# Performance work log

Hardware: AMD Instinct MI355X
Metric: run time of the kernel (lower is better)

Reference implementation:

```python
import jax, jax.numpy as jnp
import numpy as np

N = 50000      # nodes
E = 500000     # edges (before self-loops)
D_IN = 128     # embedding_dim
C = 256        # intermediate_dim (per-head out channels)
H = 1          # heads
SLOPE = 0.2    # LeakyReLU negative slope (PyG default)


def setup_inputs() -> dict:
    key = jax.random.key(0)
    ks = jax.random.split(key, 8)
    x = jax.random.normal(ks[0], (N, D_IN), dtype=jnp.float32)
    edge_index = jax.random.randint(ks[1], (2, E), 0, N, dtype=jnp.int32)
    W1 = jax.random.normal(ks[2], (H * C, D_IN), dtype=jnp.float32) / np.sqrt(D_IN)
    a1_src = jax.random.normal(ks[3], (H, C), dtype=jnp.float32) / np.sqrt(C)
    a1_dst = jax.random.normal(ks[4], (H, C), dtype=jnp.float32) / np.sqrt(C)
    b1 = jnp.zeros((C,), dtype=jnp.float32)
    W2 = jax.random.normal(ks[5], (H * C, C), dtype=jnp.float32) / np.sqrt(C)
    a2_src = jax.random.normal(ks[6], (H, C), dtype=jnp.float32) / np.sqrt(C)
    a2_dst = jax.random.normal(ks[7], (H, C), dtype=jnp.float32) / np.sqrt(C)
    b2 = jnp.zeros((C,), dtype=jnp.float32)
    return dict(x=x, edge_index=edge_index, W1=W1, a1_src=a1_src, a1_dst=a1_dst,
                b1=b1, W2=W2, a2_src=a2_src, a2_dst=a2_dst, b2=b2)


def gat_conv(x, src, dst, W, a_src, a_dst, b):
    # x: [N, Din]; W: [H*C, Din]; a_*: [H, C]; b: [C]
    h = (x @ W.T).reshape(N, H, C)                      # [N, H, C]
    e_src = jnp.einsum('nhc,hc->nh', h, a_src)          # [N, H]
    e_dst = jnp.einsum('nhc,hc->nh', h, a_dst)          # [N, H]
    e = jax.nn.leaky_relu(e_src[src] + e_dst[dst], SLOPE)  # [Etot, H]
    # segment softmax over destination nodes (self-loops guarantee >=1 edge per node)
    m = jax.lax.stop_gradient(jax.ops.segment_max(e, dst, num_segments=N))
    p = jnp.exp(e - m[dst])                             # [Etot, H]
    denom = jax.ops.segment_sum(p, dst, num_segments=N)  # [N, H]
    alpha = p / (denom[dst] + 1e-16)                    # [Etot, H]
    out = jax.ops.segment_sum(h[src] * alpha[:, :, None], dst, num_segments=N)  # [N, H, C]
    return out.mean(axis=1) + b                         # concat=False -> head mean; [N, C]


def reference(x, edge_index, W1, a1_src, a1_dst, b1, W2, a2_src, a2_dst, b2):
    # PyG GATConv default add_self_loops=True
    loop = jnp.arange(N, dtype=edge_index.dtype)
    src = jnp.concatenate([edge_index[0], loop])
    dst = jnp.concatenate([edge_index[1], loop])
    x1 = jax.nn.relu(gat_conv(x, src, dst, W1, a1_src, a1_dst, b1))
    x2 = jax.nn.relu(gat_conv(x1, src, dst, W2, a2_src, a2_dst, b2))
    return jnp.concatenate([x1, x2], axis=-1)           # [N, 2*C]
```

## Files before the change

kernel.cpp:

```cpp
#include <hip/hip_runtime.h>
#include <hip/hip_bf16.h>
#include <math.h>

#define NNODES 50000
#define NEDGES 500000
#define ETOT   (NEDGES + NNODES)
#define DIN    128
#define CH     256
#define SLOPE  0.2f

#define SCAN_TILE 1024
#define NSCAN ((NNODES + SCAN_TILE - 1) / SCAN_TILE)

typedef __attribute__((ext_vector_type(8))) short short8;
typedef __attribute__((ext_vector_type(4))) float f32x4;

static __device__ __forceinline__ float wave_reduce_max(float v) {
#pragma unroll
  for (int off = 32; off > 0; off >>= 1) v = fmaxf(v, __shfl_xor(v, off));
  return v;
}
static __device__ __forceinline__ float wave_reduce_sum(float v) {
#pragma unroll
  for (int off = 32; off > 0; off >>= 1) v += __shfl_xor(v, off);
  return v;
}

static __device__ __forceinline__ unsigned short f2bf(float f) {
  unsigned int u = __float_as_uint(f);
  unsigned int r = (u + 0x7fffu + ((u >> 16) & 1u)) >> 16;
  return (unsigned short)r;
}
static __device__ __forceinline__ float bf2f(unsigned short u) {
  return __uint_as_float(((unsigned int)u) << 16);
}

__global__ __launch_bounds__(256) void init_kernel(int* __restrict__ deg,
                                                   float* __restrict__ eS1, float* __restrict__ eD1,
                                                   float* __restrict__ eS2, float* __restrict__ eD2) {
  int i = blockIdx.x * 256 + threadIdx.x;
  if (i < NNODES) {
    deg[i] = 0;
    eS1[i] = 0.f; eD1[i] = 0.f;
    eS2[i] = 0.f; eD2[i] = 0.f;
  }
}

__global__ void degree_kernel(const int* __restrict__ ei, int* __restrict__ deg) {
  int e = blockIdx.x * blockDim.x + threadIdx.x;
  if (e >= ETOT) return;
  int dst = (e < NEDGES) ? ei[NEDGES + e] : (e - NEDGES);
  atomicAdd(&deg[dst], 1);
}

__global__ __launch_bounds__(256) void scan_blocksums(const int* __restrict__ deg,
                                                      int* __restrict__ bsums) {
  __shared__ int sdata[4];
  int b = blockIdx.x;
  int tid = threadIdx.x;
  int idx = b * SCAN_TILE + tid * 4;
  int s = 0;
  if (idx + 3 < NNODES) {
    int4 v = *(const int4*)(deg + idx);
    s = v.x + v.y + v.z + v.w;
  } else {
#pragma unroll
    for (int j = 0; j < 4; j++) if (idx + j < NNODES) s += deg[idx + j];
  }
#pragma unroll
  for (int off = 32; off > 0; off >>= 1) s += __shfl_xor(s, off);
  if ((tid & 63) == 0) sdata[tid >> 6] = s;
  __syncthreads();
  if (tid == 0) bsums[b] = sdata[0] + sdata[1] + sdata[2] + sdata[3];
}

__global__ __launch_bounds__(64) void scan_bsums(const int* __restrict__ bsums,
                                                 int* __restrict__ boffs,
                                                 int* __restrict__ rowptr) {
  int tid = threadIdx.x;
  int v = (tid < NSCAN) ? bsums[tid] : 0;
  int x = v;
#pragma unroll
  for (int off = 1; off < 64; off <<= 1) {
    int t = __shfl_up(x, off);
    if (tid >= off) x += t;
  }
  if (tid < NSCAN) boffs[tid] = x - v;
  if (tid == 63) rowptr[NNODES] = x;
}

__global__ __launch_bounds__(256) void scan_final(const int* __restrict__ deg,
                                                  const int* __restrict__ boffs,
                                                  int* __restrict__ rowptr,
                                                  int* __restrict__ cursor) {
  __shared__ int wsums[4];
  int b = blockIdx.x;
  int tid = threadIdx.x;
  int lane = tid & 63;
  int base = b * SCAN_TILE + tid * 4;
  int d[4];
  int s = 0;
#pragma unroll
  for (int j = 0; j < 4; j++) {
    d[j] = (base + j < NNODES) ? deg[base + j] : 0;
    s += d[j];
  }
  int x = s;
#pragma unroll
  for (int off = 1; off < 64; off <<= 1) {
    int t = __shfl_up(x, off);
    if (lane >= off) x += t;
  }
  if (lane == 63) wsums[tid >> 6] = x;
  __syncthreads();
  int woff = 0;
  int w = tid >> 6;
  for (int i = 0; i < w; i++) woff += wsums[i];
  int excl = boffs[b] + woff + (x - s);
#pragma unroll
  for (int j = 0; j < 4; j++) {
    if (base + j < NNODES) { rowptr[base + j] = excl; cursor[base + j] = excl; }
    excl += d[j];
  }
}

__global__ void scatter_kernel(const int* __restrict__ ei, int* __restrict__ cursor,
                               int* __restrict__ csr_src) {
  int e = blockIdx.x * blockDim.x + threadIdx.x;
  if (e >= ETOT) return;
  int src, dst;
  if (e < NEDGES) { src = ei[e]; dst = ei[NEDGES + e]; }
  else            { src = e - NEDGES; dst = src; }
  int slot = atomicAdd(&cursor[dst], 1);
  csr_src[slot] = src;
}

#define W1N4 (CH * DIN / 4)
#define W2N4 (CH * CH / 4)
__global__ __launch_bounds__(256) void cast_weights(const float* __restrict__ W1,
                                                    const float* __restrict__ W2,
                                                    unsigned short* __restrict__ Wb1,
                                                    unsigned short* __restrict__ Wb2) {
  int i = blockIdx.x * 256 + threadIdx.x;
  const float* src;
  unsigned short* dst;
  int j;
  if (i < W1N4) { src = W1; dst = Wb1; j = i; }
  else if (i < W1N4 + W2N4) { src = W2; dst = Wb2; j = i - W1N4; }
  else return;
  float4 v = *(const float4*)(src + (size_t)j * 4);
  ushort4 o;
  o.x = f2bf(v.x); o.y = f2bf(v.y); o.z = f2bf(v.z); o.w = f2bf(v.w);
  *(ushort4*)(dst + (size_t)j * 4) = o;
}

#define TM 128
#define TN 128
#define TK 64
#define LDA (TK + 8)
#define LDC (TN + 8)

__global__ __launch_bounds__(256) void gemm_bf16(
    const float* __restrict__ Xf, const unsigned short* __restrict__ Xb, int ldx,
    const unsigned short* __restrict__ W, int K,
    unsigned short* __restrict__ Hout, int M,
    const float* __restrict__ a_src, const float* __restrict__ a_dst,
    float* __restrict__ eS, float* __restrict__ eD) {
  __shared__ short smem[TM * LDA * 2];
  short* As = smem;
  short* Bs = smem + TM * LDA;
  short* Cs = smem;
  int bm = blockIdx.y * TM;
  int bn = blockIdx.x * TN;
  int tid = threadIdx.x;
  int wid = tid >> 6;
  int lane = tid & 63;
  int wm = (wid & 1) * 64;
  int wn = (wid >> 1) * 64;
  int lrow = lane & 15;
  int lk8 = (lane >> 4) * 8;

  int srow = tid >> 3;
  int skoff = (tid & 7) * 8;

  f32x4 acc[4][4] = {};

  for (int k0 = 0; k0 < K; k0 += TK) {
#pragma unroll
    for (int i = 0; i < 4; i++) {
      int r = srow + 32 * i;
      int gm = bm + r;
      short8 v = {};
      if (gm < M) {
        if (Xf) {
          const float* p = Xf + (size_t)gm * ldx + k0 + skoff;
          float4 f0 = *(const float4*)(p);
          float4 f1 = *(const float4*)(p + 4);
          v[0] = (short)f2bf(f0.x); v[1] = (short)f2bf(f0.y);
          v[2] = (short)f2bf(f0.z); v[3] = (short)f2bf(f0.w);
          v[4] = (short)f2bf(f1.x); v[5] = (short)f2bf(f1.y);
          v[6] = (short)f2bf(f1.z); v[7] = (short)f2bf(f1.w);
        } else {
          v = *(const short8*)(Xb + (size_t)gm * ldx + k0 + skoff);
        }
      }
      *(short8*)(&As[r * LDA + skoff]) = v;
      short8 w = *(const short8*)(W + (size_t)(bn + r) * K + k0 + skoff);
      *(short8*)(&Bs[r * LDA + skoff]) = w;
    }
    __syncthreads();
#pragma unroll
    for (int kk = 0; kk < TK; kk += 32) {
      short8 a[4], b[4];
#pragma unroll
      for (int mi = 0; mi < 4; mi++)
        a[mi] = *(const short8*)(&As[(wm + mi * 16 + lrow) * LDA + kk + lk8]);
#pragma unroll
      for (int ni = 0; ni < 4; ni++)
        b[ni] = *(const short8*)(&Bs[(wn + ni * 16 + lrow) * LDA + kk + lk8]);
#pragma unroll
      for (int mi = 0; mi < 4; mi++)
#pragma unroll
        for (int ni = 0; ni < 4; ni++)
          acc[mi][ni] = __builtin_amdgcn_mfma_f32_16x16x32_bf16(a[mi], b[ni], acc[mi][ni], 0, 0, 0);
    }
    __syncthreads();
  }

  int crow = (lane >> 4) * 4;
  int ccol = lane & 15;

  float asv[4], adv[4];
#pragma unroll
  for (int ni = 0; ni < 4; ni++) {
    int c = bn + wn + ni * 16 + ccol;
    asv[ni] = a_src[c];
    adv[ni] = a_dst[c];
  }
#pragma unroll
  for (int mi = 0; mi < 4; mi++) {
#pragma unroll
    for (int r = 0; r < 4; r++) {
      float s = 0.f, d = 0.f;
#pragma unroll
      for (int ni = 0; ni < 4; ni++) {
        float h = acc[mi][ni][r];
        s += h * asv[ni];
        d += h * adv[ni];
      }
#pragma unroll
      for (int off = 1; off < 16; off <<= 1) {
        s += __shfl_xor(s, off);
        d += __shfl_xor(d, off);
      }
      int gm = bm + wm + mi * 16 + crow + r;
      if (ccol == 0 && gm < M) {
        atomicAdd(&eS[gm], s);
        atomicAdd(&eD[gm], d);
      }
    }
  }

#pragma unroll
  for (int mi = 0; mi < 4; mi++) {
#pragma unroll
    for (int ni = 0; ni < 4; ni++) {
#pragma unroll
      for (int r = 0; r < 4; r++) {
        int row = wm + mi * 16 + crow + r;
        int col = wn + ni * 16 + ccol;
        Cs[row * LDC + col] = (short)f2bf(acc[mi][ni][r]);
      }
    }
  }
  __syncthreads();
  int orow = tid >> 4;
  int ocol = (tid & 15) * 8;
#pragma unroll
  for (int pp = 0; pp < 8; pp++) {
    int row = pp * 16 + orow;
    int gm = bm + row;
    if (gm < M) {
      short8 v = *(const short8*)(&Cs[row * LDC + ocol]);
      *(short8*)(&Hout[(size_t)gm * CH + bn + ocol]) = v;
    }
  }
}

__global__ __launch_bounds__(256) void aggregate_kernel(
    const unsigned short* __restrict__ Hmb, const float* __restrict__ eS,
    const float* __restrict__ eD, const int* __restrict__ rowptr,
    const int* __restrict__ csr_src, const float* __restrict__ bias,
    float* __restrict__ out, int outOffset, unsigned short* __restrict__ xout) {
  int n = blockIdx.x * 4 + (threadIdx.x >> 6);
  if (n >= NNODES) return;
  int lane = threadIdx.x & 63;
  int beg = rowptr[n], end = rowptr[n + 1];
  int deg = end - beg;
  float ed = eD[n];

  float4 acc = make_float4(0.f, 0.f, 0.f, 0.f);

  if (deg <= 64) {
    int src = 0;
    float e = -1e30f;
    if (lane < deg) {
      src = csr_src[beg + lane];
      float t = eS[src] + ed;
      e = (t >= 0.f) ? t : SLOPE * t;
    }
    float m = wave_reduce_max(e);
    float p = (lane < deg) ? __expf(e - m) : 0.f;
    float inv = 1.f / (wave_reduce_sum(p) + 1e-16f);

    for (int j0 = 0; j0 < deg; j0 += 8) {
      ushort4 hv[8];
      float al[8];
#pragma unroll
      for (int t = 0; t < 8; t++) {
        int j = j0 + t;
        int jj = (j < deg) ? j : deg - 1;
        int sj = __shfl(src, jj);
        float aj = __shfl(p, jj) * inv;
        al[t] = (j < deg) ? aj : 0.f;
        hv[t] = *(const ushort4*)(Hmb + (size_t)sj * CH + lane * 4);
      }
#pragma unroll
      for (int t = 0; t < 8; t++) {
        acc.x += al[t] * bf2f(hv[t].x);
        acc.y += al[t] * bf2f(hv[t].y);
        acc.z += al[t] * bf2f(hv[t].z);
        acc.w += al[t] * bf2f(hv[t].w);
      }
    }
  } else {
    float m = -1e30f;
    for (int i = lane; i < deg; i += 64) {
      float e = eS[csr_src[beg + i]] + ed;
      e = (e >= 0.f) ? e : SLOPE * e;
      m = fmaxf(m, e);
    }
    m = wave_reduce_max(m);
    float ds = 0.f;
    for (int i = lane; i < deg; i += 64) {
      float e = eS[csr_src[beg + i]] + ed;
      e = (e >= 0.f) ? e : SLOPE * e;
      ds += __expf(e - m);
    }
    ds = wave_reduce_sum(ds) + 1e-16f;
    float inv = 1.f / ds;
    for (int k = beg; k < end; k++) {
      int s = csr_src[k];
      float e = eS[s] + ed;
      e = (e >= 0.f) ? e : SLOPE * e;
      float alpha = __expf(e - m) * inv;
      ushort4 hu = *(const ushort4*)(Hmb + (size_t)s * CH + lane * 4);
      acc.x += alpha * bf2f(hu.x); acc.y += alpha * bf2f(hu.y);
      acc.z += alpha * bf2f(hu.z); acc.w += alpha * bf2f(hu.w);
    }
  }

  float4 b = *(const float4*)(bias + lane * 4);
  float4 o;
  o.x = fmaxf(acc.x + b.x, 0.f);
  o.y = fmaxf(acc.y + b.y, 0.f);
  o.z = fmaxf(acc.z + b.z, 0.f);
  o.w = fmaxf(acc.w + b.w, 0.f);
  *(float4*)(out + (size_t)n * 512 + outOffset + lane * 4) = o;
  if (xout) {
    ushort4 ob;
    ob.x = f2bf(o.x); ob.y = f2bf(o.y); ob.z = f2bf(o.z); ob.w = f2bf(o.w);
    *(ushort4*)(xout + (size_t)n * CH + lane * 4) = ob;
  }
}

extern "C" void kernel_launch(void* const* d_in, const int* in_sizes, int n_in,
                              void* d_out, int out_size, void* d_ws, size_t ws_size,
                              hipStream_t stream) {
  const float* x   = (const float*)d_in[0];
  const int*   ei  = (const int*)d_in[1];
  const float* W1  = (const float*)d_in[2];
  const float* a1s = (const float*)d_in[3];
  const float* a1d = (const float*)d_in[4];
  const float* b1  = (const float*)d_in[5];
  const float* W2  = (const float*)d_in[6];
  const float* a2s = (const float*)d_in[7];
  const float* a2d = (const float*)d_in[8];
  const float* b2  = (const float*)d_in[9];
  float* out = (float*)d_out;

  char* ws = (char*)d_ws;
  size_t off = 0;
  auto alloc = [&](size_t bytes) -> void* {
    void* p = ws + off;
    off = (off + bytes + 255) & ~(size_t)255;
    return p;
  };
  unsigned short* Hmb    = (unsigned short*)alloc(sizeof(short) * (size_t)NNODES * CH);
  unsigned short* Xb     = (unsigned short*)alloc(sizeof(short) * (size_t)NNODES * CH);
  unsigned short* Wb1    = (unsigned short*)alloc(sizeof(short) * CH * DIN);
  unsigned short* Wb2    = (unsigned short*)alloc(sizeof(short) * CH * CH);
  float*          eS1    = (float*)alloc(sizeof(float) * NNODES);
  float*          eD1    = (float*)alloc(sizeof(float) * NNODES);
  float*          eS2    = (float*)alloc(sizeof(float) * NNODES);
  float*          eD2    = (float*)alloc(sizeof(float) * NNODES);
  int*            rowptr = (int*)alloc(sizeof(int) * (NNODES + 1));
  int*            cursor = (int*)alloc(sizeof(int) * NNODES);
  int*            csrsrc = (int*)alloc(sizeof(int) * ETOT);
  int*            deg    = (int*)alloc(sizeof(int) * NNODES);
  int*            bsums  = (int*)alloc(sizeof(int) * NSCAN);
  int*            boffs  = (int*)alloc(sizeof(int) * NSCAN);

  init_kernel<<<(NNODES + 255) / 256, 256, 0, stream>>>(deg, eS1, eD1, eS2, eD2);
  cast_weights<<<(W1N4 + W2N4 + 255) / 256, 256, 0, stream>>>(W1, W2, Wb1, Wb2);

  degree_kernel<<<(ETOT + 255) / 256, 256, 0, stream>>>(ei, deg);
  scan_blocksums<<<NSCAN, 256, 0, stream>>>(deg, bsums);
  scan_bsums<<<1, 64, 0, stream>>>(bsums, boffs, rowptr);
  scan_final<<<NSCAN, 256, 0, stream>>>(deg, boffs, rowptr, cursor);
  scatter_kernel<<<(ETOT + 255) / 256, 256, 0, stream>>>(ei, cursor, csrsrc);

  dim3 gemm_grid(2, (NNODES + TM - 1) / TM);
  int nblk4 = (NNODES + 3) / 4;

  gemm_bf16<<<gemm_grid, 256, 0, stream>>>(x, (const unsigned short*)nullptr, DIN,
                                           Wb1, DIN, Hmb, NNODES, a1s, a1d, eS1, eD1);
  aggregate_kernel<<<nblk4, 256, 0, stream>>>(Hmb, eS1, eD1, rowptr, csrsrc, b1, out, 0, Xb);

  gemm_bf16<<<gemm_grid, 256, 0, stream>>>((const float*)nullptr, Xb, CH,
                                           Wb2, CH, Hmb, NNODES, a2s, a2d, eS2, eD2);
  aggregate_kernel<<<nblk4, 256, 0, stream>>>(Hmb, eS2, eD2, rowptr, csrsrc, b2, out, 256, (unsigned short*)nullptr);
}
```

Baseline: 335.6 us.

## Fuse init/cast and degree-count into GEMM launch; split aggregation into half-wave edges

Merges the zero-init and weight-cast kernels into one launch. It also folds the edge degree-count into the first GEMM launch as extra blocks, so the counting overlaps the GEMM and launches are removed. The aggregation kernel now has each half-wave process a different edge using 16-byte row loads of 8 bf16 channels, then combines the halves with a cross-lane shuffle. This is meant to cut gather instruction count and raise memory-level parallelism, at the cost of more registers and a final reduction.

After: 330.2 us. No clear change (-1.6%).

```diff
diff --git a/kernel.cpp b/kernel.cpp
--- a/kernel.cpp
+++ b/kernel.cpp
@@ -35,22 +35,31 @@
   return __uint_as_float(((unsigned int)u) << 16);
 }
 
-__global__ __launch_bounds__(256) void init_kernel(int* __restrict__ deg,
-                                                   float* __restrict__ eS1, float* __restrict__ eD1,
-                                                   float* __restrict__ eS2, float* __restrict__ eD2) {
+#define W1N4 (CH * DIN / 4)
+#define W2N4 (CH * CH / 4)
+__global__ __launch_bounds__(256) void init_and_cast(
+    int* __restrict__ deg,
+    float* __restrict__ eS1, float* __restrict__ eD1,
+    float* __restrict__ eS2, float* __restrict__ eD2,
+    const float* __restrict__ W1, const float* __restrict__ W2,
+    unsigned short* __restrict__ Wb1, unsigned short* __restrict__ Wb2) {
   int i = blockIdx.x * 256 + threadIdx.x;
   if (i < NNODES) {
     deg[i] = 0;
     eS1[i] = 0.f; eD1[i] = 0.f;
     eS2[i] = 0.f; eD2[i] = 0.f;
   }
-}
-
-__global__ void degree_kernel(const int* __restrict__ ei, int* __restrict__ deg) {
-  int e = blockIdx.x * blockDim.x + threadIdx.x;
-  if (e >= ETOT) return;
-  int dst = (e < NEDGES) ? ei[NEDGES + e] : (e - NEDGES);
-  atomicAdd(&deg[dst], 1);
+  if (i < W1N4 + W2N4) {
+    const float* src;
+    unsigned short* dst;
+    int j;
+    if (i < W1N4) { src = W1; dst = Wb1; j = i; }
+    else          { src = W2; dst = Wb2; j = i - W1N4; }
+    float4 v = *(const float4*)(src + (size_t)j * 4);
+    ushort4 o;
+    o.x = f2bf(v.x); o.y = f2bf(v.y); o.z = f2bf(v.z); o.w = f2bf(v.w);
+    *(ushort4*)(dst + (size_t)j * 4) = o;
+  }
 }
 
 __global__ __launch_bounds__(256) void scan_blocksums(const int* __restrict__ deg,
@@ -135,43 +144,25 @@
   csr_src[slot] = src;
 }
 
-#define W1N4 (CH * DIN / 4)
-#define W2N4 (CH * CH / 4)
-__global__ __launch_bounds__(256) void cast_weights(const float* __restrict__ W1,
-                                                    const float* __restrict__ W2,
-                                                    unsigned short* __restrict__ Wb1,
-                                                    unsigned short* __restrict__ Wb2) {
-  int i = blockIdx.x * 256 + threadIdx.x;
-  const float* src;
-  unsigned short* dst;
-  int j;
-  if (i < W1N4) { src = W1; dst = Wb1; j = i; }
-  else if (i < W1N4 + W2N4) { src = W2; dst = Wb2; j = i - W1N4; }
-  else return;
-  float4 v = *(const float4*)(src + (size_t)j * 4);
-  ushort4 o;
-  o.x = f2bf(v.x); o.y = f2bf(v.y); o.z = f2bf(v.z); o.w = f2bf(v.w);
-  *(ushort4*)(dst + (size_t)j * 4) = o;
-}
-
 #define TM 128
 #define TN 128
 #define TK 64
 #define LDA (TK + 8)
 #define LDC (TN + 8)
-
-__global__ __launch_bounds__(256) void gemm_bf16(
+#define GEMM_GRID (2 * ((NNODES + TM - 1) / TM))
+#define DEG_BLOCKS ((ETOT + 255) / 256)
+
+static __device__ __forceinline__ void gemm_body(
     const float* __restrict__ Xf, const unsigned short* __restrict__ Xb, int ldx,
     const unsigned short* __restrict__ W, int K,
     unsigned short* __restrict__ Hout, int M,
     const float* __restrict__ a_src, const float* __restrict__ a_dst,
-    float* __restrict__ eS, float* __restrict__ eD) {
+    float* __restrict__ eS, float* __restrict__ eD,
+    int bm, int bn) {
   __shared__ short smem[TM * LDA * 2];
   short* As = smem;
   short* Bs = smem + TM * LDA;
   short* Cs = smem;
-  int bm = blockIdx.y * TM;
-  int bn = blockIdx.x * TN;
   int tid = threadIdx.x;
   int wid = tid >> 6;
   int lane = tid & 63;
@@ -287,6 +278,37 @@
   }
 }
 
+__global__ __launch_bounds__(256) void gemm1_deg(
+    const float* __restrict__ Xf, const unsigned short* __restrict__ W,
+    unsigned short* __restrict__ Hout,
+    const float* __restrict__ a_src, const float* __restrict__ a_dst,
+    float* __restrict__ eS, float* __restrict__ eD,
+    const int* __restrict__ ei, int* __restrict__ deg) {
+  if (blockIdx.x >= GEMM_GRID) {
+    int e = (blockIdx.x - GEMM_GRID) * 256 + threadIdx.x;
+    if (e < ETOT) {
+      int dst = (e < NEDGES) ? ei[NEDGES + e] : (e - NEDGES);
+      atomicAdd(&deg[dst], 1);
+    }
+    return;
+  }
+  int bn = (blockIdx.x & 1) * TN;
+  int bm = (blockIdx.x >> 1) * TM;
+  gemm_body(Xf, (const unsigned short*)nullptr, DIN, W, DIN, Hout, NNODES,
+            a_src, a_dst, eS, eD, bm, bn);
+}
+
+__global__ __launch_bounds__(256) void gemm_l2(
+    const unsigned short* __restrict__ Xb, const unsigned short* __restrict__ W,
+    unsigned short* __restrict__ Hout,
+    const float* __restrict__ a_src, const float* __restrict__ a_dst,
+    float* __restrict__ eS, float* __restrict__ eD) {
+  int bn = blockIdx.x * TN;
+  int bm = blockIdx.y * TM;
+  gemm_body((const float*)nullptr, Xb, CH, W, CH, Hout, NNODES,
+            a_src, a_dst, eS, eD, bm, bn);
+}
+
 __global__ __launch_bounds__(256) void aggregate_kernel(
     const unsigned short* __restrict__ Hmb, const float* __restrict__ eS,
     const float* __restrict__ eD, const int* __restrict__ rowptr,
@@ -295,11 +317,15 @@
   int n = blockIdx.x * 4 + (threadIdx.x >> 6);
   if (n >= NNODES) return;
   int lane = threadIdx.x & 63;
+  int half = lane >> 5;
+  int cg = lane & 31;
   int beg = rowptr[n], end = rowptr[n + 1];
   int deg = end - beg;
   float ed = eD[n];
 
-  float4 acc = make_float4(0.f, 0.f, 0.f, 0.f);
+  float acc8[8];
+#pragma unroll
+  for (int k = 0; k < 8; k++) acc8[k] = 0.f;
 
   if (deg <= 64) {
     int src = 0;
@@ -312,25 +338,30 @@
     float m = wave_reduce_max(e);
     float p = (lane < deg) ? __expf(e - m) : 0.f;
     float inv = 1.f / (wave_reduce_sum(p) + 1e-16f);
-
-    for (int j0 = 0; j0 < deg; j0 += 8) {
-      ushort4 hv[8];
+    float av = p * inv;
+
+    for (int j0 = 0; j0 < deg; j0 += 16) {
+      uint4 hv[8];
       float al[8];
 #pragma unroll
       for (int t = 0; t < 8; t++) {
-        int j = j0 + t;
+        int j = j0 + 2 * t + half;
         int jj = (j < deg) ? j : deg - 1;
         int sj = __shfl(src, jj);
-        float aj = __shfl(p, jj) * inv;
+        float aj = __shfl(av, jj);
         al[t] = (j < deg) ? aj : 0.f;
-        hv[t] = *(const ushort4*)(Hmb + (size_t)sj * CH + lane * 4);
+        hv[t] = *(const uint4*)(Hmb + (size_t)sj * CH + cg * 8);
       }
 #pragma unroll
       for (int t = 0; t < 8; t++) {
-        acc.x += al[t] * bf2f(hv[t].x);
-        acc.y += al[t] * bf2f(hv[t].y);
-        acc.z += al[t] * bf2f(hv[t].z);
-        acc.w += al[t] * bf2f(hv[t].w);
+        acc8[0] += al[t] * __uint_as_float(hv[t].x << 16);
+        acc8[1] += al[t] * __uint_as_float(hv[t].x & 0xffff0000u);
+        acc8[2] += al[t] * __uint_as_float(hv[t].y << 16);
+        acc8[3] += al[t] * __uint_as_float(hv[t].y & 0xffff0000u);
+        acc8[4] += al[t] * __uint_as_float(hv[t].z << 16);
+        acc8[5] += al[t] * __uint_as_float(hv[t].z & 0xffff0000u);
+        acc8[6] += al[t] * __uint_as_float(hv[t].w << 16);
+        acc8[7] += al[t] * __uint_as_float(hv[t].w & 0xffff0000u);
       }
     }
   } else {
@@ -347,30 +378,45 @@
       e = (e >= 0.f) ? e : SLOPE * e;
       ds += __expf(e - m);
     }
-    ds = wave_reduce_sum(ds) + 1e-16f;
-    float inv = 1.f / ds;
-    for (int k = beg; k < end; k++) {
+    float inv = 1.f / (wave_reduce_sum(ds) + 1e-16f);
+    for (int j = 0; j < deg; j += 2) {
+      int jj = j + half;
+      int k = beg + ((jj < deg) ? jj : deg - 1);
       int s = csr_src[k];
       float e = eS[s] + ed;
       e = (e >= 0.f) ? e : SLOPE * e;
-      float alpha = __expf(e - m) * inv;
-      ushort4 hu = *(const ushort4*)(Hmb + (size_t)s * CH + lane * 4);
-      acc.x += alpha * bf2f(hu.x); acc.y += alpha * bf2f(hu.y);
-      acc.z += alpha * bf2f(hu.z); acc.w += alpha * bf2f(hu.w);
-    }
-  }
-
-  float4 b = *(const float4*)(bias + lane * 4);
+      float alpha = (jj < deg) ? __expf(e - m) * inv : 0.f;
+      uint4 u = *(const uint4*)(Hmb + (size_t)s * CH + cg * 8);
+      acc8[0] += alpha * __uint_as_float(u.x << 16);
+      acc8[1] += alpha * __uint_as_float(u.x & 0xffff0000u);
+      acc8[2] += alpha * __uint_as_float(u.y << 16);
+      acc8[3] += alpha * __uint_as_float(u.y & 0xffff0000u);
+      acc8[4] += alpha * __uint_as_float(u.z << 16);
+      acc8[5] += alpha * __uint_as_float(u.z & 0xffff0000u);
+      acc8[6] += alpha * __uint_as_float(u.w << 16);
+      acc8[7] += alpha * __uint_as_float(u.w & 0xffff0000u);
+    }
+  }
+
+#pragma unroll
+  for (int k = 0; k < 8; k++) acc8[k] += __shfl_xor(acc8[k], 32);
+
+  float a0 = half ? acc8[4] : acc8[0];
+  float a1 = half ? acc8[5] : acc8[1];
+  float a2 = half ? acc8[6] : acc8[2];
+  float a3 = half ? acc8[7] : acc8[3];
+  int cbase = cg * 8 + half * 4;
+  float4 b = *(const float4*)(bias + cbase);
   float4 o;
-  o.x = fmaxf(acc.x + b.x, 0.f);
-  o.y = fmaxf(acc.y + b.y, 0.f);
-  o.z = fmaxf(acc.z + b.z, 0.f);
-  o.w = fmaxf(acc.w + b.w, 0.f);
-  *(float4*)(out + (size_t)n * 512 + outOffset + lane * 4) = o;
+  o.x = fmaxf(a0 + b.x, 0.f);
+  o.y = fmaxf(a1 + b.y, 0.f);
+  o.z = fmaxf(a2 + b.z, 0.f);
+  o.w = fmaxf(a3 + b.w, 0.f);
+  *(float4*)(out + (size_t)n * 512 + outOffset + cbase) = o;
   if (xout) {
     ushort4 ob;
     ob.x = f2bf(o.x); ob.y = f2bf(o.y); ob.z = f2bf(o.z); ob.w = f2bf(o.w);
-    *(ushort4*)(xout + (size_t)n * CH + lane * 4) = ob;
+    *(ushort4*)(xout + (size_t)n * CH + cbase) = ob;
   }
 }
 
@@ -411,23 +457,22 @@
   int*            bsums  = (int*)alloc(sizeof(int) * NSCAN);
   int*            boffs  = (int*)alloc(sizeof(int) * NSCAN);
 
-  init_kernel<<<(NNODES + 255) / 256, 256, 0, stream>>>(deg, eS1, eD1, eS2, eD2);
-  cast_weights<<<(W1N4 + W2N4 + 255) / 256, 256, 0, stream>>>(W1, W2, Wb1, Wb2);
-
-  degree_kernel<<<(ETOT + 255) / 256, 256, 0, stream>>>(ei, deg);
+  int nblk4 = (NNODES + 3) / 4;
+
+  init_and_cast<<<(NNODES + 255) / 256, 256, 0, stream>>>(deg, eS1, eD1, eS2, eD2,
+                                                          W1, W2, Wb1, Wb2);
+
+  gemm1_deg<<<GEMM_GRID + DEG_BLOCKS, 256, 0, stream>>>(x, Wb1, Hmb, a1s, a1d,
+                                                        eS1, eD1, ei, deg);
+
   scan_blocksums<<<NSCAN, 256, 0, stream>>>(deg, bsums);
   scan_bsums<<<1, 64, 0, stream>>>(bsums, boffs, rowptr);
   scan_final<<<NSCAN, 256, 0, stream>>>(deg, boffs, rowptr, cursor);
   scatter_kernel<<<(ETOT + 255) / 256, 256, 0, stream>>>(ei, cursor, csrsrc);
 
-  dim3 gemm_grid(2, (NNODES + TM - 1) / TM);
-  int nblk4 = (NNODES + 3) / 4;
-
-  gemm_bf16<<<gemm_grid, 256, 0, stream>>>(x, (const unsigned short*)nullptr, DIN,
-                                           Wb1, DIN, Hmb, NNODES, a1s, a1d, eS1, eD1);
   aggregate_kernel<<<nblk4, 256, 0, stream>>>(Hmb, eS1, eD1, rowptr, csrsrc, b1, out, 0, Xb);
 
-  gemm_bf16<<<gemm_grid, 256, 0, stream>>>((const float*)nullptr, Xb, CH,
-                                           Wb2, CH, Hmb, NNODES, a2s, a2d, eS2, eD2);
-  aggregate_kernel<<<nblk4, 256, 0, stream>>>(Hmb, eS2, eD2, rowptr, csrsrc, b2, out, 256, (unsigned short*)nullptr);
-}
+  gemm_l2<<<dim3(2, (NNODES + TM - 1) / TM), 256, 0, stream>>>(Xb, Wb2, Hmb, a2s, a2d, eS2, eD2);
+  aggregate_kernel<<<nblk4, 256, 0, stream>>>(Hmb, eS2, eD2, rowptr, csrsrc, b2, out, 256,
+                                              (unsigned short*)nullptr);
+}
```
